# Kernel optimization log

Hardware: AMD Instinct MI355X
Metric: run time of the kernel (lower is better)

Reference implementation:

```python
import jax, jax.numpy as jnp
import numpy as np

N, DIM, R, C = 1024, 201, 72, 4


def setup_inputs() -> dict:
    key = jax.random.key(0)
    k1, k2 = jax.random.split(key)
    x = jax.random.normal(k1, (N, DIM, R, C), dtype=jnp.float32)
    labels = jax.random.randint(k2, (N, R, C), 0, 201, dtype=jnp.int64)
    return {"x": x, "labels": labels}


def _parse_top_down(labels, G):
    # Faithful vectorization of the triple python loop:
    #   top  = first row index with a valid label (label < G); empty if none
    #   down = 0 if rows 0->1 is a valid->invalid transition,
    #          else R-1 if last row valid,
    #          else first valid->invalid transition index; empty if no valid row.
    # (top empty <=> down empty <=> no valid row; then both forced to 0)
    R = labels.shape[1]
    valid = labels < G                              # [n, R, C]
    any_valid = valid.any(axis=1)                   # [n, C]
    first_valid = jnp.argmax(valid, axis=1)         # [n, C]
    trans = valid[:, :-1] & ~valid[:, 1:]           # [n, R-1, C] valid->invalid
    any_trans = trans.any(axis=1)
    first_trans = jnp.argmax(trans, axis=1)
    down = jnp.where(trans[:, 0], 0,
                     jnp.where(valid[:, -1], R - 1,
                               jnp.where(any_trans, first_trans, 0)))
    top = jnp.where(any_valid, first_valid, 0)
    down = jnp.where(any_valid, down, 0)
    return top, down                                # [n, C] each


def _lane_loss(x, labels):
    n, dim, R, C = x.shape
    G = dim - 1
    # softmax-weighted expected grid position per (image, row, lane)
    p = jax.nn.softmax(x[:, :G], axis=1)
    emb = jnp.arange(G, dtype=x.dtype).reshape(1, G, 1, 1)
    pos = jnp.sum(p * emb, axis=1)                  # [n, R, C]

    top, down = _parse_top_down(labels, G)

    # second difference across lanes: d_i - d_{i+1} = pos_i - 2 pos_{i+1} + pos_{i+2}
    dd = jnp.abs(pos[:, :, :-2] - 2.0 * pos[:, :, 1:-1] + pos[:, :, 2:])  # [n, R, C-2]
    rows = jnp.arange(R)

    def side(lane_lo, lane_hi, col_lo, col_hi):
        t = jnp.max(top[:, lane_lo:lane_hi], axis=1)   # [n]
        d = jnp.min(down[:, lane_lo:lane_hi], axis=1)  # [n]
        active = t < d
        W = (d - t + 1).astype(x.dtype)                # segment length
        mask = ((rows[None, :] >= t[:, None]) & (rows[None, :] <= d[:, None])).astype(x.dtype)
        s = jnp.einsum('nr,nrc->n', mask, dd[:, :, col_lo:col_hi])
        Wsafe = jnp.where(active, W, 1.0)
        npairs = float(col_hi - col_lo)                # == C-3 pairs of diffs
        # L1 mean over W rows, then /W again, then / (num pairs)
        loss = jnp.where(active, s / (Wsafe * Wsafe) / npairs, 0.0)
        w = jnp.where(active, W, 0.0)
        return loss, w, active

    loss_l, w_l, left = side(0, 3, 0, C - 3)
    loss_r, w_r, right = side(1, 4, 1, C - 2)
    denom = jnp.where(left & right, 2.0 * R, float(R))
    loss_k = (loss_l * w_l + loss_r * w_r) / denom     # [n]
    flag = jnp.sum((loss_k != 0).astype(jnp.int32))
    total = jnp.sum(loss_k)
    return jnp.where(flag > 0, total / flag.astype(x.dtype), jnp.asarray(0.0, x.dtype))


def reference(x, labels):
    return _lane_loss(x, labels)
```

## Files before the change

### kernel.cpp

```cpp
#include <hip/hip_runtime.h>

#define NIMG  1024
#define DIMX  201
#define GVAL  200
#define RROW  72
#define CLN   4
#define COLS  (RROW * CLN)
#define NSL   4
#define NGRP  (COLS / 4)

__global__ __launch_bounds__(COLS) void lane_loss_main(
    const float* __restrict__ x, const int* __restrict__ labels,
    float* __restrict__ total, int* __restrict__ flag)
{
    __shared__ float s_lds[NSL][COLS];
    __shared__ float w_lds[NSL][COLS];
    __shared__ float pos_s[COLS];
    __shared__ unsigned char valid_s[COLS];
    __shared__ int td_s[8];

    const int n   = blockIdx.x;
    const int tid = threadIdx.x;

    {
        int lab = labels[n * COLS + tid];
        valid_s[tid] = (lab < GVAL) ? 1 : 0;
    }

    const int slice = tid / NGRP;
    const int g     = tid - slice * NGRP;

    const float* xp = x + (size_t)n * (DIMX * COLS) + g * 4;
    float4 sa = make_float4(0.f, 0.f, 0.f, 0.f);
    float4 wa = make_float4(0.f, 0.f, 0.f, 0.f);
    float df = (float)slice;
    #pragma unroll 5
    for (int d = slice; d < GVAL; d += NSL) {
        float4 v = *(const float4*)(xp + (size_t)d * COLS);
        float ex = __expf(v.x), ey = __expf(v.y),
              ez = __expf(v.z), ew = __expf(v.w);
        sa.x += ex;              sa.y += ey;
        sa.z += ez;              sa.w += ew;
        wa.x = fmaf(df, ex, wa.x); wa.y = fmaf(df, ey, wa.y);
        wa.z = fmaf(df, ez, wa.z); wa.w = fmaf(df, ew, wa.w);
        df += (float)NSL;
    }
    ((float4*)s_lds[slice])[g] = sa;
    ((float4*)w_lds[slice])[g] = wa;
    __syncthreads();

    {
        float st = s_lds[0][tid] + s_lds[1][tid] + s_lds[2][tid] + s_lds[3][tid];
        float wt = w_lds[0][tid] + w_lds[1][tid] + w_lds[2][tid] + w_lds[3][tid];
        pos_s[tid] = wt / st;
    }
    __syncthreads();

    if (tid < CLN) {
        const int c = tid;
        bool any_valid = false; int first_valid = 0;
        bool any_trans = false; int first_trans = 0;
        bool trans0 = false;
        bool v_prev = (valid_s[c] != 0);
        if (v_prev) { any_valid = true; first_valid = 0; }
        for (int r = 1; r < RROW; ++r) {
            bool v = (valid_s[r * CLN + c] != 0);
            if (v && !any_valid) { any_valid = true; first_valid = r; }
            bool tr = v_prev && !v;
            if (tr && !any_trans) { any_trans = true; first_trans = r - 1; }
            if (r == 1) trans0 = tr;
            v_prev = v;
        }
        bool valid_last = v_prev;
        int down;
        if (trans0)          down = 0;
        else if (valid_last) down = RROW - 1;
        else if (any_trans)  down = first_trans;
        else                 down = 0;
        int top = any_valid ? first_valid : 0;
        if (!any_valid) down = 0;
        td_s[c]     = top;
        td_s[4 + c] = down;
    }
    __syncthreads();

    if (tid < 64) {
        const int t_l = max(td_s[0], max(td_s[1], td_s[2]));
        const int d_l = min(td_s[4], min(td_s[5], td_s[6]));
        const int t_r = max(td_s[1], max(td_s[2], td_s[3]));
        const int d_r = min(td_s[5], min(td_s[6], td_s[7]));

        float sl = 0.f, sr = 0.f;
        for (int r = tid; r < RROW; r += 64) {
            float p0 = pos_s[r * 4 + 0];
            float p1 = pos_s[r * 4 + 1];
            float p2 = pos_s[r * 4 + 2];
            float p3 = pos_s[r * 4 + 3];
            float ddl = fabsf(p0 - 2.f * p1 + p2);
            float ddr = fabsf(p1 - 2.f * p2 + p3);
            if (r >= t_l && r <= d_l) sl += ddl;
            if (r >= t_r && r <= d_r) sr += ddr;
        }
        #pragma unroll
        for (int off = 32; off > 0; off >>= 1) {
            sl += __shfl_down(sl, off, 64);
            sr += __shfl_down(sr, off, 64);
        }
        if (tid == 0) {
            bool aL = (t_l < d_l), aR = (t_r < d_r);
            float WL = (float)(d_l - t_l + 1);
            float WR = (float)(d_r - t_r + 1);
            float ll = aL ? (sl / WL) : 0.f;
            float lr = aR ? (sr / WR) : 0.f;
            float denom = (aL && aR) ? (2.f * (float)RROW) : (float)RROW;
            float lk = (ll + lr) / denom;
            if (lk != 0.f) {
                atomicAdd(total, lk);
                atomicAdd(flag, 1);
            }
        }
    }
}

__global__ void lane_loss_finalize(const float* __restrict__ total,
                                   const int* __restrict__ flag,
                                   float* __restrict__ out)
{
    if (blockIdx.x == 0 && threadIdx.x == 0) {
        int f = *flag;
        out[0] = (f > 0) ? (*total / (float)f) : 0.f;
    }
}

extern "C" void kernel_launch(void* const* d_in, const int* in_sizes, int n_in,
                              void* d_out, int out_size, void* d_ws, size_t ws_size,
                              hipStream_t stream)
{
    const float* x      = (const float*)d_in[0];
    const int*   labels = (const int*)d_in[1];
    float*       out    = (float*)d_out;

    float* total = (float*)d_ws;
    int*   flag  = (int*)((char*)d_ws + sizeof(float));

    hipMemsetAsync(d_ws, 0, 2 * sizeof(float), stream);

    lane_loss_main<<<NIMG, COLS, 0, stream>>>(x, labels, total, flag);
    lane_loss_finalize<<<1, 64, 0, stream>>>(total, flag, out);
}
```

Baseline: 328.2 us.

## Skip softmax over rows outside active segments and fuse finalize via done counter

Label parsing now runs first to compute the union of the active row ranges for the left and right sides. Only those rows have their softmax-weighted positions computed, and inactive images skip the x loads entirely. The separate finalize kernel is replaced by a last-block-done atomic counter inside the main kernel, removing one launch. The trade-off is serialized label parsing before the memory-bound loads and data-dependent thread counts.

```diff
diff --git a/kernel.cpp b/kernel.cpp
--- a/kernel.cpp
+++ b/kernel.cpp
@@ -7,11 +7,11 @@
 #define CLN   4
 #define COLS  (RROW * CLN)
 #define NSL   4
-#define NGRP  (COLS / 4)
 
 __global__ __launch_bounds__(COLS) void lane_loss_main(
     const float* __restrict__ x, const int* __restrict__ labels,
-    float* __restrict__ total, int* __restrict__ flag)
+    float* __restrict__ total, int* __restrict__ flag,
+    int* __restrict__ done, float* __restrict__ out)
 {
     __shared__ float s_lds[NSL][COLS];
     __shared__ float w_lds[NSL][COLS];
@@ -22,38 +22,7 @@
     const int n   = blockIdx.x;
     const int tid = threadIdx.x;
 
-    {
-        int lab = labels[n * COLS + tid];
-        valid_s[tid] = (lab < GVAL) ? 1 : 0;
-    }
-
-    const int slice = tid / NGRP;
-    const int g     = tid - slice * NGRP;
-
-    const float* xp = x + (size_t)n * (DIMX * COLS) + g * 4;
-    float4 sa = make_float4(0.f, 0.f, 0.f, 0.f);
-    float4 wa = make_float4(0.f, 0.f, 0.f, 0.f);
-    float df = (float)slice;
-    #pragma unroll 5
-    for (int d = slice; d < GVAL; d += NSL) {
-        float4 v = *(const float4*)(xp + (size_t)d * COLS);
-        float ex = __expf(v.x), ey = __expf(v.y),
-              ez = __expf(v.z), ew = __expf(v.w);
-        sa.x += ex;              sa.y += ey;
-        sa.z += ez;              sa.w += ew;
-        wa.x = fmaf(df, ex, wa.x); wa.y = fmaf(df, ey, wa.y);
-        wa.z = fmaf(df, ez, wa.z); wa.w = fmaf(df, ew, wa.w);
-        df += (float)NSL;
-    }
-    ((float4*)s_lds[slice])[g] = sa;
-    ((float4*)w_lds[slice])[g] = wa;
-    __syncthreads();
-
-    {
-        float st = s_lds[0][tid] + s_lds[1][tid] + s_lds[2][tid] + s_lds[3][tid];
-        float wt = w_lds[0][tid] + w_lds[1][tid] + w_lds[2][tid] + w_lds[3][tid];
-        pos_s[tid] = wt / st;
-    }
+    valid_s[tid] = (labels[n * COLS + tid] < GVAL) ? 1 : 0;
     __syncthreads();
 
     if (tid < CLN) {
@@ -84,51 +53,90 @@
     }
     __syncthreads();
 
-    if (tid < 64) {
-        const int t_l = max(td_s[0], max(td_s[1], td_s[2]));
-        const int d_l = min(td_s[4], min(td_s[5], td_s[6]));
-        const int t_r = max(td_s[1], max(td_s[2], td_s[3]));
-        const int d_r = min(td_s[5], min(td_s[6], td_s[7]));
+    const int t_l = max(td_s[0], max(td_s[1], td_s[2]));
+    const int d_l = min(td_s[4], min(td_s[5], td_s[6]));
+    const int t_r = max(td_s[1], max(td_s[2], td_s[3]));
+    const int d_r = min(td_s[5], min(td_s[6], td_s[7]));
+    const bool aL = (t_l < d_l), aR = (t_r < d_r);
 
-        float sl = 0.f, sr = 0.f;
-        for (int r = tid; r < RROW; r += 64) {
-            float p0 = pos_s[r * 4 + 0];
-            float p1 = pos_s[r * 4 + 1];
-            float p2 = pos_s[r * 4 + 2];
-            float p3 = pos_s[r * 4 + 3];
-            float ddl = fabsf(p0 - 2.f * p1 + p2);
-            float ddr = fabsf(p1 - 2.f * p2 + p3);
-            if (r >= t_l && r <= d_l) sl += ddl;
-            if (r >= t_r && r <= d_r) sr += ddr;
+    int rmin = RROW, rmax = -1;
+    if (aL) { rmin = t_l; rmax = d_l; }
+    if (aR) { rmin = min(rmin, t_r); rmax = max(rmax, d_r); }
+
+    if (rmax >= 0) {
+        const int ngroups = rmax - rmin + 1;
+        const int nact    = NSL * ngroups;
+
+        if (tid < nact) {
+            const int slice = tid / ngroups;
+            const int g     = tid - slice * ngroups;
+            const float* xp = x + (size_t)n * (DIMX * COLS) + (size_t)(rmin + g) * CLN;
+            float4 sa = make_float4(0.f, 0.f, 0.f, 0.f);
+            float4 wa = make_float4(0.f, 0.f, 0.f, 0.f);
+            float df = (float)slice;
+            #pragma unroll 10
+            for (int d = slice; d < GVAL; d += NSL) {
+                float4 v = *(const float4*)(xp + (size_t)d * COLS);
+                float ex = __expf(v.x), ey = __expf(v.y),
+                      ez = __expf(v.z), ew = __expf(v.w);
+                sa.x += ex;                sa.y += ey;
+                sa.z += ez;                sa.w += ew;
+                wa.x = fmaf(df, ex, wa.x); wa.y = fmaf(df, ey, wa.y);
+                wa.z = fmaf(df, ez, wa.z); wa.w = fmaf(df, ew, wa.w);
+                df += (float)NSL;
+            }
+            ((float4*)s_lds[slice])[g] = sa;
+            ((float4*)w_lds[slice])[g] = wa;
         }
-        #pragma unroll
-        for (int off = 32; off > 0; off >>= 1) {
-            sl += __shfl_down(sl, off, 64);
-            sr += __shfl_down(sr, off, 64);
+        __syncthreads();
+
+        if (tid < nact) {
+            float st = s_lds[0][tid] + s_lds[1][tid] + s_lds[2][tid] + s_lds[3][tid];
+            float wt = w_lds[0][tid] + w_lds[1][tid] + w_lds[2][tid] + w_lds[3][tid];
+            pos_s[tid] = wt / st;
         }
-        if (tid == 0) {
-            bool aL = (t_l < d_l), aR = (t_r < d_r);
-            float WL = (float)(d_l - t_l + 1);
-            float WR = (float)(d_r - t_r + 1);
-            float ll = aL ? (sl / WL) : 0.f;
-            float lr = aR ? (sr / WR) : 0.f;
-            float denom = (aL && aR) ? (2.f * (float)RROW) : (float)RROW;
-            float lk = (ll + lr) / denom;
-            if (lk != 0.f) {
-                atomicAdd(total, lk);
-                atomicAdd(flag, 1);
+        __syncthreads();
+
+        if (tid < 64) {
+            float sl = 0.f, sr = 0.f;
+            for (int r = rmin + tid; r <= rmax; r += 64) {
+                const int lr_ = r - rmin;
+                float p0 = pos_s[lr_ * 4 + 0];
+                float p1 = pos_s[lr_ * 4 + 1];
+                float p2 = pos_s[lr_ * 4 + 2];
+                float p3 = pos_s[lr_ * 4 + 3];
+                float ddl = fabsf(p0 - 2.f * p1 + p2);
+                float ddr = fabsf(p1 - 2.f * p2 + p3);
+                if (r >= t_l && r <= d_l) sl += ddl;
+                if (r >= t_r && r <= d_r) sr += ddr;
+            }
+            #pragma unroll
+            for (int off = 32; off > 0; off >>= 1) {
+                sl += __shfl_down(sl, off, 64);
+                sr += __shfl_down(sr, off, 64);
+            }
+            if (tid == 0) {
+                float WL = (float)(d_l - t_l + 1);
+                float WR = (float)(d_r - t_r + 1);
+                float ll = aL ? (sl / WL) : 0.f;
+                float lr = aR ? (sr / WR) : 0.f;
+                float denom = (aL && aR) ? (2.f * (float)RROW) : (float)RROW;
+                float lk = (ll + lr) / denom;
+                if (lk != 0.f) {
+                    atomicAdd(total, lk);
+                    atomicAdd(flag, 1);
+                }
             }
         }
     }
-}
 
-__global__ void lane_loss_finalize(const float* __restrict__ total,
-                                   const int* __restrict__ flag,
-                                   float* __restrict__ out)
-{
-    if (blockIdx.x == 0 && threadIdx.x == 0) {
-        int f = *flag;
-        out[0] = (f > 0) ? (*total / (float)f) : 0.f;
+    if (tid == 0) {
+        __threadfence();
+        if (atomicAdd(done, 1) == NIMG - 1) {
+            float tot = atomicAdd(total, 0.f);
+            int   f   = atomicAdd(flag, 0);
+            out[0] = (f > 0) ? (tot / (float)f) : 0.f;
+        }
     }
 }
 
@@ -142,9 +150,9 @@
 
     float* total = (float*)d_ws;
     int*   flag  = (int*)((char*)d_ws + sizeof(float));
+    int*   done  = (int*)((char*)d_ws + 2 * sizeof(float));
 
-    hipMemsetAsync(d_ws, 0, 2 * sizeof(float), stream);
+    hipMemsetAsync(d_ws, 0, 3 * sizeof(float), stream);
 
-    lane_loss_main<<<NIMG, COLS, 0, stream>>>(x, labels, total, flag);
-    lane_loss_finalize<<<1, 64, 0, stream>>>(total, flag, out);
+    lane_loss_main<<<NIMG, COLS, 0, stream>>>(x, labels, total, flag, done, out);
 }
```

Measured after the change: 368.3 us. 1.12x slower.

## Software-pipeline nontemporal x loads and fuse finalize via last-block atomic counter

Applied to the files above, without the earlier changes.

The softmax-position loop is fully unrolled and keeps an 8-deep register ring of prefetched nontemporal float4 loads, so more memory requests are in flight per thread. Launch bounds now request 4 blocks per CU. The separate finalize kernel is removed: the last block to finish, detected with an atomic done counter after a threadfence, computes the final mean. This cuts one kernel launch but adds register pressure from the prefetch buffer.

```diff
diff --git a/kernel.cpp b/kernel.cpp
--- a/kernel.cpp
+++ b/kernel.cpp
@@ -8,10 +8,15 @@
 #define COLS  (RROW * CLN)
 #define NSL   4
 #define NGRP  (COLS / 4)
+#define NIT   (GVAL / NSL)
+#define PIPE  8
 
-__global__ __launch_bounds__(COLS) void lane_loss_main(
+typedef float vfloat4 __attribute__((ext_vector_type(4)));
+
+__global__ __launch_bounds__(COLS, 4) void lane_loss_main(
     const float* __restrict__ x, const int* __restrict__ labels,
-    float* __restrict__ total, int* __restrict__ flag)
+    float* __restrict__ total, int* __restrict__ flag,
+    int* __restrict__ done, float* __restrict__ out)
 {
     __shared__ float s_lds[NSL][COLS];
     __shared__ float w_lds[NSL][COLS];
@@ -22,25 +27,32 @@
     const int n   = blockIdx.x;
     const int tid = threadIdx.x;
 
-    {
-        int lab = labels[n * COLS + tid];
-        valid_s[tid] = (lab < GVAL) ? 1 : 0;
-    }
+    valid_s[tid] = (labels[n * COLS + tid] < GVAL) ? 1 : 0;
 
     const int slice = tid / NGRP;
     const int g     = tid - slice * NGRP;
 
-    const float* xp = x + (size_t)n * (DIMX * COLS) + g * 4;
+    const float* xp = x + (size_t)n * (DIMX * COLS) + (size_t)slice * COLS + g * 4;
+
+    vfloat4 v[PIPE];
+    #pragma unroll
+    for (int j = 0; j < PIPE; ++j)
+        v[j] = __builtin_nontemporal_load((const vfloat4*)(xp + (size_t)j * (4 * COLS)));
+
     float4 sa = make_float4(0.f, 0.f, 0.f, 0.f);
     float4 wa = make_float4(0.f, 0.f, 0.f, 0.f);
     float df = (float)slice;
-    #pragma unroll 5
-    for (int d = slice; d < GVAL; d += NSL) {
-        float4 v = *(const float4*)(xp + (size_t)d * COLS);
-        float ex = __expf(v.x), ey = __expf(v.y),
-              ez = __expf(v.z), ew = __expf(v.w);
-        sa.x += ex;              sa.y += ey;
-        sa.z += ez;              sa.w += ew;
+
+    #pragma unroll
+    for (int i = 0; i < NIT; ++i) {
+        vfloat4 cur = v[i & (PIPE - 1)];
+        if (i + PIPE < NIT)
+            v[i & (PIPE - 1)] = __builtin_nontemporal_load(
+                (const vfloat4*)(xp + (size_t)(i + PIPE) * (4 * COLS)));
+        float ex = __expf(cur.x), ey = __expf(cur.y),
+              ez = __expf(cur.z), ew = __expf(cur.w);
+        sa.x += ex;                sa.y += ey;
+        sa.z += ez;                sa.w += ew;
         wa.x = fmaf(df, ex, wa.x); wa.y = fmaf(df, ey, wa.y);
         wa.z = fmaf(df, ez, wa.z); wa.w = fmaf(df, ew, wa.w);
         df += (float)NSL;
@@ -64,12 +76,12 @@
         bool v_prev = (valid_s[c] != 0);
         if (v_prev) { any_valid = true; first_valid = 0; }
         for (int r = 1; r < RROW; ++r) {
-            bool v = (valid_s[r * CLN + c] != 0);
-            if (v && !any_valid) { any_valid = true; first_valid = r; }
-            bool tr = v_prev && !v;
+            bool vv = (valid_s[r * CLN + c] != 0);
+            if (vv && !any_valid) { any_valid = true; first_valid = r; }
+            bool tr = v_prev && !vv;
             if (tr && !any_trans) { any_trans = true; first_trans = r - 1; }
             if (r == 1) trans0 = tr;
-            v_prev = v;
+            v_prev = vv;
         }
         bool valid_last = v_prev;
         int down;
@@ -120,15 +132,14 @@
             }
         }
     }
-}
 
-__global__ void lane_loss_finalize(const float* __restrict__ total,
-                                   const int* __restrict__ flag,
-                                   float* __restrict__ out)
-{
-    if (blockIdx.x == 0 && threadIdx.x == 0) {
-        int f = *flag;
-        out[0] = (f > 0) ? (*total / (float)f) : 0.f;
+    if (tid == 0) {
+        __threadfence();
+        if (atomicAdd(done, 1) == NIMG - 1) {
+            float tot = atomicAdd(total, 0.f);
+            int   f   = atomicAdd(flag, 0);
+            out[0] = (f > 0) ? (tot / (float)f) : 0.f;
+        }
     }
 }
 
@@ -141,10 +152,10 @@
     float*       out    = (float*)d_out;
 
     float* total = (float*)d_ws;
-    int*   flag  = (int*)((char*)d_ws + sizeof(float));
+    int*   flag  = (int*)((char*)d_ws + 4);
+    int*   done  = (int*)((char*)d_ws + 8);
 
-    hipMemsetAsync(d_ws, 0, 2 * sizeof(float), stream);
+    (void)hipMemsetAsync(d_ws, 0, 12, stream);
 
-    lane_loss_main<<<NIMG, COLS, 0, stream>>>(x, labels, total, flag);
-    lane_loss_finalize<<<1, 64, 0, stream>>>(total, flag, out);
+    lane_loss_main<<<NIMG, COLS, 0, stream>>>(x, labels, total, flag, done, out);
 }
```

After: 344.3 us. +4.9%, slower.
